# Kernel optimization log

Measured on AMD Instinct MI355X. Metric: run time of the kernel, lower is better.

Reference implementation:

```python
import jax, jax.numpy as jnp
import numpy as np

MARGIN = 0.5

def _pairwise_dist(x):
    # Euclidean cdist with grad-safe sqrt (diagonal is exactly zero).
    sq = jnp.sum(x * x, axis=1)
    d2 = sq[:, None] + sq[None, :] - 2.0 * (x @ x.T)
    d2 = jnp.maximum(d2, 0.0)
    safe = jnp.where(d2 > 0.0, d2, 1.0)
    return jnp.where(d2 > 0.0, jnp.sqrt(safe), 0.0)

def setup_inputs() -> dict:
    key = jax.random.key(0)
    k1, k2 = jax.random.split(key)
    embeddings = jax.random.normal(k1, (8192, 128), dtype=jnp.float32)
    labels = jax.random.randint(k2, (8192,), 0, 256, dtype=jnp.int64)
    return {"embeddings": embeddings, "labels": labels}

def reference(embeddings, labels):
    B = embeddings.shape[0]
    dist = _pairwise_dist(embeddings)                      # [B, B]
    same = labels[:, None] == labels[None, :]              # [B, B]
    eye = jnp.eye(B, dtype=bool)
    pos_mask = same & ~eye
    neg_mask = ~same
    neg_inf = jnp.float32(-jnp.inf)
    pos_inf = jnp.float32(jnp.inf)
    hardest_pos = jnp.max(jnp.where(pos_mask, dist, neg_inf), axis=1)  # [B]
    hardest_neg = jnp.min(jnp.where(neg_mask, dist, pos_inf), axis=1)  # [B]
    valid = jnp.any(pos_mask, axis=1) & jnp.any(neg_mask, axis=1)      # [B]
    per_anchor = jnp.maximum(hardest_pos - hardest_neg + MARGIN, 0.0)
    per_anchor = jnp.where(valid, per_anchor, 0.0)
    num = jnp.sum(valid.astype(jnp.float32))
    return jnp.sum(per_anchor) / jnp.maximum(num, 1.0)
```

## Files before the change

### kernel.cpp

```cpp
#include <hip/hip_runtime.h>
#include <hip/hip_bf16.h>
#include <stdint.h>


typedef __bf16 bf16x8 __attribute__((ext_vector_type(8)));
typedef float f32x4 __attribute__((ext_vector_type(4)));

constexpr int NB = 8192;
constexpr int ND = 128;
constexpr int SPLIT = 16;
constexpr int JR = NB / SPLIT;
constexpr int BN = 64;
constexpr int NT = JR / BN;
constexpr int BM = 128;
constexpr int NRB = NB / BM;

constexpr size_t OFF_XB  = 0;
constexpr size_t OFF_XM2 = (size_t)NB * ND * 2;
constexpr size_t OFF_SQ  = OFF_XM2 + (size_t)NB * ND * 2;
constexpr size_t OFF_LAB = OFF_SQ + (size_t)NB * 4;
constexpr size_t OFF_HP  = OFF_LAB + (size_t)NB * 4;
constexpr size_t OFF_HN  = OFF_HP + (size_t)SPLIT * NB * 4;
constexpr size_t OFF_ACC = OFF_HN + (size_t)SPLIT * NB * 4;

__device__ __forceinline__ unsigned short f2bf(float f) {
  union { float f; uint32_t u; } c; c.f = f;
  uint32_t u = c.u;
  u += 0x7fffu + ((u >> 16) & 1u);
  return (unsigned short)(u >> 16);
}

__global__ __launch_bounds__(256) void prep_kernel(
    const float* __restrict__ x, const int* __restrict__ labels,
    unsigned short* __restrict__ xb, unsigned short* __restrict__ xm2,
    float* __restrict__ sq, int* __restrict__ lab,
    float* __restrict__ acc, int* __restrict__ cnt) {
  if (blockIdx.x == 0 && threadIdx.x == 0) {
    acc[0] = 0.f;
    acc[1] = 0.f;
    *cnt = 0;
  }
  const int row = blockIdx.x * 8 + (threadIdx.x >> 5);
  const int sub = threadIdx.x & 31;
  const float4 v = *reinterpret_cast<const float4*>(x + (size_t)row * ND + sub * 4);
  ushort4 o, o2;
  o.x = f2bf(v.x); o.y = f2bf(v.y); o.z = f2bf(v.z); o.w = f2bf(v.w);
  o2.x = f2bf(-2.f * v.x); o2.y = f2bf(-2.f * v.y);
  o2.z = f2bf(-2.f * v.z); o2.w = f2bf(-2.f * v.w);
  *reinterpret_cast<ushort4*>(xb + (size_t)row * ND + sub * 4) = o;
  *reinterpret_cast<ushort4*>(xm2 + (size_t)row * ND + sub * 4) = o2;
  float s = v.x * v.x + v.y * v.y + v.z * v.z + v.w * v.w;
#pragma unroll
  for (int m = 1; m < 32; m <<= 1) s += __shfl_xor(s, m);
  if (sub == 0) {
    sq[row] = s;
    lab[row] = labels[row];
  }
}

__global__ __launch_bounds__(256, 4) void hard_kernel(
    const unsigned short* __restrict__ xb, const unsigned short* __restrict__ xm2,
    const float* __restrict__ sq, const int* __restrict__ lab,
    float* __restrict__ hp_out, float* __restrict__ hn_out) {
  __shared__ __align__(16) char smem[2][BN * ND * 2];
  __shared__ float sql[JR];
  __shared__ int labl[JR];
  const int tid = threadIdx.x;
  const int lane = tid & 63;
  const int w = tid >> 6;
  const int c16 = lane & 15;
  const int g4 = lane >> 4;
  const int rowbase = blockIdx.x * BM + w * 32;
  const int colbase = blockIdx.y * JR;

  auto stage = [&](int buf, int tile) {
    const char* gbase = reinterpret_cast<const char*>(xb) +
                        ((size_t)(colbase + tile * BN)) * (ND * 2);
#pragma unroll
    for (int rnd = 0; rnd < 4; ++rnd) {
      const int L = rnd * 4096 + tid * 16;
      const int slot = (L >> 4) & 15;
      const int col = L >> 8;
      const int src = (L & ~0xF0) | ((slot ^ (col & 15)) << 4);
      __builtin_amdgcn_global_load_lds(
          (const __attribute__((address_space(1))) unsigned int*)(gbase + src),
          (__attribute__((address_space(3))) unsigned int*)(&smem[buf][L]),
          16, 0, 0);
    }
  };

  stage(0, 0);
  {
    const int i2 = tid * 2;
    *reinterpret_cast<float2*>(&sql[i2]) =
        *reinterpret_cast<const float2*>(&sq[colbase + i2]);
    *reinterpret_cast<int2*>(&labl[i2]) =
        *reinterpret_cast<const int2*>(&lab[colbase + i2]);
  }

  bf16x8 afrag[2][4];
#pragma unroll
  for (int rt = 0; rt < 2; ++rt) {
    const unsigned short* ap =
        xm2 + ((size_t)(rowbase + rt * 16 + c16)) * ND + g4 * 8;
#pragma unroll
    for (int kk = 0; kk < 4; ++kk)
      afrag[rt][kk] = *reinterpret_cast<const bf16x8*>(ap + kk * 32);
  }
  int labr[2][4];
#pragma unroll
  for (int rt = 0; rt < 2; ++rt)
#pragma unroll
    for (int rr = 0; rr < 4; ++rr)
      labr[rt][rr] = lab[rowbase + rt * 16 + g4 * 4 + rr];

  float hp2[2][4], hn2[2][4];
#pragma unroll
  for (int rt = 0; rt < 2; ++rt)
#pragma unroll
    for (int rr = 0; rr < 4; ++rr) {
      hp2[rt][rr] = -__builtin_inff();
      hn2[rt][rr] = __builtin_inff();
    }

  __syncthreads();

  for (int t = 0; t < NT; ++t) {
    if (t + 1 < NT) stage((t + 1) & 1, t + 1);
    const char* sb = smem[t & 1];
#pragma unroll
    for (int jj = 0; jj < 4; ++jj) {
      const int colL = jj * 16 + c16;
      const int jidx = t * BN + colL;
      const float sqc = sql[jidx];
      const int labc = labl[jidx];

      bf16x8 bfrag[4];
#pragma unroll
      for (int kk = 0; kk < 4; ++kk) {
        const int kbyte = kk * 64 + g4 * 16;
        const int a = colL * 256 + (kbyte ^ (c16 << 4));
        bfrag[kk] = *reinterpret_cast<const bf16x8*>(sb + a);
      }

      f32x4 acc[2];
#pragma unroll
      for (int rt = 0; rt < 2; ++rt) acc[rt] = (f32x4){sqc, sqc, sqc, sqc};
#pragma unroll
      for (int kk = 0; kk < 4; ++kk)
#pragma unroll
        for (int rt = 0; rt < 2; ++rt)
          acc[rt] = __builtin_amdgcn_mfma_f32_16x16x32_bf16(
              afrag[rt][kk], bfrag[kk], acc[rt], 0, 0, 0);

#pragma unroll
      for (int rt = 0; rt < 2; ++rt)
#pragma unroll
        for (int rr = 0; rr < 4; ++rr) {
          const float tv = acc[rt][rr];
          const bool same = (labc == labr[rt][rr]);
          hp2[rt][rr] = fmaxf(hp2[rt][rr], same ? tv : -__builtin_inff());
          hn2[rt][rr] = fminf(hn2[rt][rr], same ? __builtin_inff() : tv);
        }
    }
    __syncthreads();
  }

#pragma unroll
  for (int rt = 0; rt < 2; ++rt)
#pragma unroll
    for (int rr = 0; rr < 4; ++rr) {
      float p = hp2[rt][rr], n = hn2[rt][rr];
#pragma unroll
      for (int m = 1; m <= 8; m <<= 1) {
        p = fmaxf(p, __shfl_xor(p, m));
        n = fminf(n, __shfl_xor(n, m));
      }
      if (c16 == 0) {
        const int rg = rowbase + rt * 16 + g4 * 4 + rr;
        hp_out[(size_t)blockIdx.y * NB + rg] = p;
        hn_out[(size_t)blockIdx.y * NB + rg] = n;
      }
    }
}

__global__ __launch_bounds__(256) void reduce_kernel(
    const float* __restrict__ hp, const float* __restrict__ hn,
    const float* __restrict__ sq, float* __restrict__ acc,
    int* __restrict__ cnt_done, float* __restrict__ out) {
  const int a = blockIdx.x * 256 + threadIdx.x;
  float p = -__builtin_inff(), n = __builtin_inff();
#pragma unroll
  for (int s = 0; s < SPLIT; ++s) {
    p = fmaxf(p, hp[(size_t)s * NB + a]);
    n = fminf(n, hn[(size_t)s * NB + a]);
  }
  const float sqa = sq[a];
  const float d2p = fmaxf(sqa + p, 0.f);
  const float d2n = fmaxf(sqa + n, 0.f);
  const bool valid = (d2p > 1.0f) && (n < 1e37f);
  float loss = valid ? fmaxf(sqrtf(d2p) - sqrtf(d2n) + 0.5f, 0.f) : 0.f;
  float c = valid ? 1.f : 0.f;
#pragma unroll
  for (int m = 1; m < 64; m <<= 1) {
    loss += __shfl_xor(loss, m);
    c += __shfl_xor(c, m);
  }
  __shared__ float ls[4], cs[4];
  const int w = threadIdx.x >> 6, lane = threadIdx.x & 63;
  if (lane == 0) { ls[w] = loss; cs[w] = c; }
  __syncthreads();
  if (threadIdx.x == 0) {
    atomicAdd(&acc[0], ls[0] + ls[1] + ls[2] + ls[3]);
    atomicAdd(&acc[1], cs[0] + cs[1] + cs[2] + cs[3]);
    __threadfence();
    const int old = atomicAdd(cnt_done, 1);
    if (old == (NB / 256) - 1) {
      const float l = atomicAdd(&acc[0], 0.0f);
      const float nvalid = atomicAdd(&acc[1], 0.0f);
      out[0] = l / fmaxf(nvalid, 1.f);
    }
  }
}

extern "C" void kernel_launch(void* const* d_in, const int* in_sizes, int n_in,
                              void* d_out, int out_size, void* d_ws,
                              size_t ws_size, hipStream_t stream) {
  const float* x = (const float*)d_in[0];
  const int* labels = (const int*)d_in[1];
  char* ws = (char*)d_ws;
  unsigned short* xb = (unsigned short*)(ws + OFF_XB);
  unsigned short* xm2 = (unsigned short*)(ws + OFF_XM2);
  float* sq = (float*)(ws + OFF_SQ);
  int* lab = (int*)(ws + OFF_LAB);
  float* hp = (float*)(ws + OFF_HP);
  float* hn = (float*)(ws + OFF_HN);
  float* acc = (float*)(ws + OFF_ACC);
  int* cnt = (int*)(ws + OFF_ACC + 8);

  prep_kernel<<<NB / 8, 256, 0, stream>>>(x, labels, xb, xm2, sq, lab, acc, cnt);
  hard_kernel<<<dim3(NRB, SPLIT), 256, 0, stream>>>(xb, xm2, sq, lab, hp, hn);
  reduce_kernel<<<NB / 256, 256, 0, stream>>>(hp, hn, sq, acc, cnt,
                                              (float*)d_out);
}
```

Baseline: 88.92 us.

## Sort anchors by label and skip label masking on disjoint tiles

Adds a single-block counting sort that groups samples by label, then permutes the embeddings into that order during the bf16 prep pass. Because labels are now sorted, each 16-column chunk can be compared against a warp's row-label range. When the ranges cannot overlap, the chunk takes a cheap negatives-only min update with no per-element label compares. The price is an extra serial one-block kernel launch and a gather in prep. The final loss is order-invariant, so the permutation does not change the result.

```diff
diff --git a/kernel.cpp b/kernel.cpp
--- a/kernel.cpp
+++ b/kernel.cpp
@@ -8,6 +8,7 @@
 
 constexpr int NB = 8192;
 constexpr int ND = 128;
+constexpr int NCLS = 256;
 constexpr int SPLIT = 16;
 constexpr int JR = NB / SPLIT;
 constexpr int BN = 64;
@@ -19,7 +20,8 @@
 constexpr size_t OFF_XM2 = (size_t)NB * ND * 2;
 constexpr size_t OFF_SQ  = OFF_XM2 + (size_t)NB * ND * 2;
 constexpr size_t OFF_LAB = OFF_SQ + (size_t)NB * 4;
-constexpr size_t OFF_HP  = OFF_LAB + (size_t)NB * 4;
+constexpr size_t OFF_IDX = OFF_LAB + (size_t)NB * 4;
+constexpr size_t OFF_HP  = OFF_IDX + (size_t)NB * 4;
 constexpr size_t OFF_HN  = OFF_HP + (size_t)SPLIT * NB * 4;
 constexpr size_t OFF_ACC = OFF_HN + (size_t)SPLIT * NB * 4;
 
@@ -30,32 +32,60 @@
   return (unsigned short)(u >> 16);
 }
 
+__global__ __launch_bounds__(1024) void sort_kernel(
+    const int* __restrict__ labels, int* __restrict__ sortIdx,
+    int* __restrict__ labS, float* __restrict__ acc, int* __restrict__ cnt) {
+  __shared__ int hist[NCLS];
+  __shared__ int base[NCLS];
+  const int tid = threadIdx.x;
+  if (tid == 0) { acc[0] = 0.f; acc[1] = 0.f; *cnt = 0; }
+  if (tid < NCLS) hist[tid] = 0;
+  __syncthreads();
+  int myl[8];
+#pragma unroll
+  for (int k = 0; k < 8; ++k) {
+    myl[k] = labels[k * 1024 + tid];
+    atomicAdd(&hist[myl[k]], 1);
+  }
+  __syncthreads();
+  if (tid < NCLS) base[tid] = hist[tid];
+  __syncthreads();
+  for (int d = 1; d < NCLS; d <<= 1) {
+    int v = 0;
+    if (tid < NCLS && tid >= d) v = base[tid - d];
+    __syncthreads();
+    if (tid < NCLS) base[tid] += v;
+    __syncthreads();
+  }
+  if (tid < NCLS) base[tid] -= hist[tid];
+  __syncthreads();
+#pragma unroll
+  for (int k = 0; k < 8; ++k) {
+    const int i = k * 1024 + tid;
+    const int pos = atomicAdd(&base[myl[k]], 1);
+    sortIdx[pos] = i;
+    labS[pos] = myl[k];
+  }
+}
+
 __global__ __launch_bounds__(256) void prep_kernel(
-    const float* __restrict__ x, const int* __restrict__ labels,
+    const float* __restrict__ x, const int* __restrict__ sortIdx,
     unsigned short* __restrict__ xb, unsigned short* __restrict__ xm2,
-    float* __restrict__ sq, int* __restrict__ lab,
-    float* __restrict__ acc, int* __restrict__ cnt) {
-  if (blockIdx.x == 0 && threadIdx.x == 0) {
-    acc[0] = 0.f;
-    acc[1] = 0.f;
-    *cnt = 0;
-  }
-  const int row = blockIdx.x * 8 + (threadIdx.x >> 5);
+    float* __restrict__ sq) {
+  const int srow = blockIdx.x * 8 + (threadIdx.x >> 5);
   const int sub = threadIdx.x & 31;
-  const float4 v = *reinterpret_cast<const float4*>(x + (size_t)row * ND + sub * 4);
+  const int orig = sortIdx[srow];
+  const float4 v = *reinterpret_cast<const float4*>(x + (size_t)orig * ND + sub * 4);
   ushort4 o, o2;
   o.x = f2bf(v.x); o.y = f2bf(v.y); o.z = f2bf(v.z); o.w = f2bf(v.w);
   o2.x = f2bf(-2.f * v.x); o2.y = f2bf(-2.f * v.y);
   o2.z = f2bf(-2.f * v.z); o2.w = f2bf(-2.f * v.w);
-  *reinterpret_cast<ushort4*>(xb + (size_t)row * ND + sub * 4) = o;
-  *reinterpret_cast<ushort4*>(xm2 + (size_t)row * ND + sub * 4) = o2;
+  *reinterpret_cast<ushort4*>(xb + (size_t)srow * ND + sub * 4) = o;
+  *reinterpret_cast<ushort4*>(xm2 + (size_t)srow * ND + sub * 4) = o2;
   float s = v.x * v.x + v.y * v.y + v.z * v.z + v.w * v.w;
 #pragma unroll
   for (int m = 1; m < 32; m <<= 1) s += __shfl_xor(s, m);
-  if (sub == 0) {
-    sq[row] = s;
-    lab[row] = labels[row];
-  }
+  if (sub == 0) sq[srow] = s;
 }
 
 __global__ __launch_bounds__(256, 4) void hard_kernel(
@@ -73,6 +103,9 @@
   const int rowbase = blockIdx.x * BM + w * 32;
   const int colbase = blockIdx.y * JR;
 
+  const int rlo = lab[rowbase];
+  const int rhi = lab[rowbase + 31];
+
   auto stage = [&](int buf, int tile) {
     const char* gbase = reinterpret_cast<const char*>(xb) +
                         ((size_t)(colbase + tile * BN)) * (ND * 2);
@@ -130,10 +163,9 @@
     const char* sb = smem[t & 1];
 #pragma unroll
     for (int jj = 0; jj < 4; ++jj) {
+      const int g0 = t * BN + jj * 16;
       const int colL = jj * 16 + c16;
-      const int jidx = t * BN + colL;
-      const float sqc = sql[jidx];
-      const int labc = labl[jidx];
+      const float sqc = sql[g0 + c16];
 
       bf16x8 bfrag[4];
 #pragma unroll
@@ -153,15 +185,26 @@
           acc[rt] = __builtin_amdgcn_mfma_f32_16x16x32_bf16(
               afrag[rt][kk], bfrag[kk], acc[rt], 0, 0, 0);
 
-#pragma unroll
-      for (int rt = 0; rt < 2; ++rt)
-#pragma unroll
-        for (int rr = 0; rr < 4; ++rr) {
-          const float tv = acc[rt][rr];
-          const bool same = (labc == labr[rt][rr]);
-          hp2[rt][rr] = fmaxf(hp2[rt][rr], same ? tv : -__builtin_inff());
-          hn2[rt][rr] = fminf(hn2[rt][rr], same ? __builtin_inff() : tv);
-        }
+      const int clo = labl[g0];
+      const int chi = labl[g0 + 15];
+      if (clo > rhi || chi < rlo) {
+#pragma unroll
+        for (int rt = 0; rt < 2; ++rt)
+#pragma unroll
+          for (int rr = 0; rr < 4; ++rr)
+            hn2[rt][rr] = fminf(hn2[rt][rr], acc[rt][rr]);
+      } else {
+        const int labc = labl[g0 + c16];
+#pragma unroll
+        for (int rt = 0; rt < 2; ++rt)
+#pragma unroll
+          for (int rr = 0; rr < 4; ++rr) {
+            const float tv = acc[rt][rr];
+            const bool same = (labc == labr[rt][rr]);
+            hp2[rt][rr] = fmaxf(hp2[rt][rr], same ? tv : -__builtin_inff());
+            hn2[rt][rr] = fminf(hn2[rt][rr], same ? __builtin_inff() : tv);
+          }
+      }
     }
     __syncthreads();
   }
@@ -233,12 +276,14 @@
   unsigned short* xm2 = (unsigned short*)(ws + OFF_XM2);
   float* sq = (float*)(ws + OFF_SQ);
   int* lab = (int*)(ws + OFF_LAB);
+  int* sidx = (int*)(ws + OFF_IDX);
   float* hp = (float*)(ws + OFF_HP);
   float* hn = (float*)(ws + OFF_HN);
   float* acc = (float*)(ws + OFF_ACC);
   int* cnt = (int*)(ws + OFF_ACC + 8);
 
-  prep_kernel<<<NB / 8, 256, 0, stream>>>(x, labels, xb, xm2, sq, lab, acc, cnt);
+  sort_kernel<<<1, 1024, 0, stream>>>(labels, sidx, lab, acc, cnt);
+  prep_kernel<<<NB / 8, 256, 0, stream>>>(x, sidx, xb, xm2, sq);
   hard_kernel<<<dim3(NRB, SPLIT), 256, 0, stream>>>(xb, xm2, sq, lab, hp, hn);
   reduce_kernel<<<NB / 256, 256, 0, stream>>>(hp, hn, sq, acc, cnt,
                                               (float*)d_out);
```

After: 101.9 us. 14.6% more time.
